# Performance work log

Hardware: AMD Instinct MI355X
Metric: run time of the kernel (lower is better)

The kernel has to match this reference:

```python
import jax, jax.numpy as jnp
import numpy as np

N_NODES = 20000
N_EDGES = 320000
IN_DIM = 256
OUT_DIM = 256
NUM_RELS = 8
NUM_BASES = 4


def setup_inputs() -> dict:
    key = jax.random.key(0)
    k = jax.random.split(key, 7)
    return {
        "h": jax.random.normal(k[0], (N_NODES, IN_DIM), dtype=jnp.float32),
        "basis": jax.random.normal(k[1], (NUM_BASES, IN_DIM, OUT_DIM), dtype=jnp.float32)
        * (6.0 / (IN_DIM + OUT_DIM)) ** 0.5,
        "w_comp": jax.random.normal(k[2], (NUM_RELS, NUM_BASES), dtype=jnp.float32),
        "bias": jax.random.normal(k[3], (OUT_DIM,), dtype=jnp.float32) * 0.01,
        "src": jax.random.randint(k[4], (N_EDGES,), 0, N_NODES, dtype=jnp.int32),
        "dst": jax.random.randint(k[5], (N_EDGES,), 0, N_NODES, dtype=jnp.int32),
        "etype": jax.random.randint(k[6], (N_EDGES,), 0, NUM_RELS, dtype=jnp.int32),
    }


def reference(h, basis, w_comp, bias, src, dst, etype):
    # Faithful to the torch basis-decomposition quirk:
    #   weight.view(in, B, out); matmul(w_comp, .) -> [in, R, out]; view -> [R, in, out]
    in_dim, out_dim = h.shape[1], basis.shape[2]
    num_rels = w_comp.shape[0]
    wr = basis.reshape(in_dim, NUM_BASES, out_dim)          # raw-buffer reinterpret (torch .view)
    weight = jnp.einsum("rb,ibo->iro", w_comp, wr)          # [in, R, out]
    weight = weight.reshape(num_rels, in_dim, out_dim)      # raw-buffer reinterpret (torch .view)

    # msg_e = h[src_e] @ weight[etype_e]. Group by relation: transform all nodes
    # under every relation weight (dense GEMMs), then gather per edge.
    t = jnp.einsum("nd,rdo->rno", h, weight)                # [R, N, out]
    msg = t[etype, src]                                     # [E, out]

    # scatter-sum aggregation to destination nodes (dgl fn.sum)
    agg = jax.ops.segment_sum(msg, dst, num_segments=h.shape[0])  # [N, out]
    return jax.nn.relu(agg + bias)
```

## Files before the change

kernel.cpp:

```cpp
#include <hip/hip_runtime.h>


#define N_NODES  20000
#define N_EDGES  320000
#define IN_DIM   256
#define OUT_DIM  256
#define NUM_RELS 8
#define KDIM     128
#define M_PAD    20032
#define CAP      96

#define FOLD_BLOCKS 2500
#define FILL_BLOCKS 1250
#define BP_BLOCKS   128

typedef __attribute__((ext_vector_type(8)))  short short8;
typedef __attribute__((ext_vector_type(16))) float float16v;

static __device__ __forceinline__ unsigned f2bf_rne(float x) {
    unsigned u = __float_as_uint(x);
    return (u + 0x7fffu + ((u >> 16) & 1u)) >> 16;
}
static __device__ __forceinline__ float bf2f(unsigned b) {
    return __uint_as_float(b << 16);
}

__global__ __launch_bounds__(256)
void prep_kernel(const float* __restrict__ h, const float* __restrict__ w_comp,
                 unsigned short* __restrict__ U,
                 const int* __restrict__ src, const int* __restrict__ dst,
                 const int* __restrict__ et,
                 int* __restrict__ cnt, int* __restrict__ bucket,
                 const float* __restrict__ basis, unsigned short* __restrict__ Bp) {
    int b = blockIdx.x;
    int t = threadIdx.x;
    if (b < FOLD_BLOCKS) {
        int gid = b * 256 + t;
        int n = gid >> 5, k = gid & 31;
        const float* hp = h + (size_t)n * IN_DIM + k * 8;
        float4 h0 = *(const float4*)hp;
        float4 h1 = *(const float4*)(hp + 4);
        float hv[8] = {h0.x, h0.y, h0.z, h0.w, h1.x, h1.y, h1.z, h1.w};
        float a0 = 0.f, a1 = 0.f, a2 = 0.f, a3 = 0.f;
#pragma unroll
        for (int j = 0; j < 8; ++j) {
            float hj = hv[j];
            a0 += hj * w_comp[j * 4 + 0];
            a1 += hj * w_comp[j * 4 + 1];
            a2 += hj * w_comp[j * 4 + 2];
            a3 += hj * w_comp[j * 4 + 3];
        }
        uint2 p;
        p.x = f2bf_rne(a0) | (f2bf_rne(a1) << 16);
        p.y = f2bf_rne(a2) | (f2bf_rne(a3) << 16);
        *(uint2*)(U + ((size_t)n << 7) + k * 4) = p;
    } else if (b < FOLD_BLOCKS + FILL_BLOCKS) {
        int e = (b - FOLD_BLOCKS) * 256 + t;
        int d = dst[e];
        int p = atomicAdd(&cnt[d], 1);
        if (p < CAP) bucket[(size_t)d * CAP + p] = src[e] | (et[e] << 16);
    } else {
        int frag = (b - FOLD_BLOCKS - FILL_BLOCKS) * 256 + t;
        int lane = frag & 63;
        int ks   = (frag >> 6) & 7;
        int r    = (frag >> 9) & 7;
        int ct   = frag >> 12;
        int o  = ct * 32 + (lane & 31);
        int kb = r * 128 + ks * 16 + (lane >> 5) * 8;
        const float* bsp = basis + (size_t)kb * 256 + o;
        unsigned v[8];
#pragma unroll
        for (int j = 0; j < 8; ++j) v[j] = f2bf_rne(bsp[(size_t)j * 256]);
        uint4 p;
        p.x = v[0] | (v[1] << 16);
        p.y = v[2] | (v[3] << 16);
        p.z = v[4] | (v[5] << 16);
        p.w = v[6] | (v[7] << 16);
        *(uint4*)(Bp + (size_t)frag * 8) = p;
    }
}

__global__ __launch_bounds__(256)
void aggregate_kernel(const unsigned short* __restrict__ U,
                      const int* __restrict__ cnt,
                      const int* __restrict__ bucket,
                      unsigned int* __restrict__ S) {
    int wid  = threadIdx.x >> 6;
    int lane = threadIdx.x & 63;
    int d = blockIdx.x * 4 + wid;
    float2 acc[NUM_RELS];
#pragma unroll
    for (int r = 0; r < NUM_RELS; ++r) { acc[r].x = 0.f; acc[r].y = 0.f; }

    if (d < N_NODES) {
        int n = cnt[d];
        if (n > CAP) n = CAP;
        const int4* bp4 = (const int4*)(bucket + (size_t)d * CAP);
        int4 e4 = bp4[0];
        for (int i = 0; i < n; i += 4) {
            int4 cur = e4;
            e4 = bp4[(i >> 2) + 1];
            int m = n - i;
            int es[4] = {cur.x, cur.y, cur.z, cur.w};
#pragma unroll
            for (int j = 0; j < 4; ++j) {
                if (j < m) {
                    int e = es[j];
                    int s = e & 0xffff;
                    int r = __builtin_amdgcn_readfirstlane(e >> 16);
                    unsigned u = *(const unsigned*)(U + ((size_t)s << 7) + lane * 2);
                    float fx = bf2f(u & 0xffffu), fy = bf2f(u >> 16);
                    switch (r) {
                        case 0: acc[0].x += fx; acc[0].y += fy; break;
                        case 1: acc[1].x += fx; acc[1].y += fy; break;
                        case 2: acc[2].x += fx; acc[2].y += fy; break;
                        case 3: acc[3].x += fx; acc[3].y += fy; break;
                        case 4: acc[4].x += fx; acc[4].y += fy; break;
                        case 5: acc[5].x += fx; acc[5].y += fy; break;
                        case 6: acc[6].x += fx; acc[6].y += fy; break;
                        default: acc[7].x += fx; acc[7].y += fy; break;
                    }
                }
            }
        }
    }
#pragma unroll
    for (int r = 0; r < NUM_RELS; ++r) {
        unsigned p = f2bf_rne(acc[r].x) | (f2bf_rne(acc[r].y) << 16);
        S[(((size_t)r * M_PAD + d) << 6) + lane] = p;
    }
}

__global__ __launch_bounds__(512)
void gemm_kernel(const unsigned short* __restrict__ S,
                 const unsigned short* __restrict__ Bp,
                 const float* __restrict__ bias,
                 float* __restrict__ out) {
    __shared__ unsigned short At[32][136];
    int t = threadIdx.x;
    int w = t >> 6, lane = t & 63;
    int ln = lane & 31, hi = lane >> 5;
    int n0 = blockIdx.x * 32;
    int c0 = w * 32;

    int srow = t >> 4, sq = t & 15;
    const unsigned short* sbase = S + (((size_t)n0 + srow) << 7) + sq * 8;
    uint4 pre = *(const uint4*)sbase;

    float16v acc = {};

    for (int r = 0; r < NUM_RELS; ++r) {
        if (r > 0) __syncthreads();
        *(uint4*)&At[srow][sq * 8] = pre;
        __syncthreads();
        if (r + 1 < NUM_RELS)
            pre = *(const uint4*)(sbase + (((size_t)(r + 1) * M_PAD) << 7));
        const unsigned short* bpr = Bp + (((size_t)(w * 8 + r) * 8) << 9) + lane * 8;
#pragma unroll
        for (int ks = 0; ks < 8; ++ks) {
            short8 a  = *(const short8*)&At[ln][ks * 16 + hi * 8];
            short8 bo = *(const short8*)(bpr + (ks << 9));
            acc = __builtin_amdgcn_mfma_f32_32x32x16_bf16(a, bo, acc, 0, 0, 0);
        }
    }

    float bs = bias[c0 + ln];
#pragma unroll
    for (int reg = 0; reg < 16; ++reg) {
        int row = (reg & 3) + 8 * (reg >> 2) + 4 * hi;
        int n = n0 + row;
        if (n < N_NODES)
            out[(size_t)n * OUT_DIM + c0 + ln] = fmaxf(acc[reg] + bs, 0.f);
    }
}

extern "C" void kernel_launch(void* const* d_in, const int* in_sizes, int n_in,
                              void* d_out, int out_size, void* d_ws, size_t ws_size,
                              hipStream_t stream) {
    const float* h      = (const float*)d_in[0];
    const float* basis  = (const float*)d_in[1];
    const float* w_comp = (const float*)d_in[2];
    const float* bias   = (const float*)d_in[3];
    const int*   src    = (const int*)d_in[4];
    const int*   dst    = (const int*)d_in[5];
    const int*   etype  = (const int*)d_in[6];
    float*       out    = (float*)d_out;

    char* ws = (char*)d_ws;
    size_t off = 0;
    unsigned short* U   = (unsigned short*)(ws + off); off += (size_t)N_NODES * KDIM * 2;
    unsigned int*   S   = (unsigned int*)(ws + off);   off += (size_t)NUM_RELS * M_PAD * KDIM * 2;
    unsigned short* Bp  = (unsigned short*)(ws + off); off += (size_t)8 * 8 * 8 * 64 * 8 * 2;
    int* cnt    = (int*)(ws + off); off += (size_t)M_PAD * 4;
    int* bucket = (int*)(ws + off); off += ((size_t)M_PAD * CAP + 16) * 4;

    hipMemsetAsync(cnt, 0, (size_t)N_NODES * 4, stream);

    prep_kernel<<<FOLD_BLOCKS + FILL_BLOCKS + BP_BLOCKS, 256, 0, stream>>>(
        h, w_comp, U, src, dst, etype, cnt, bucket, basis, Bp);

    aggregate_kernel<<<M_PAD / 4, 256, 0, stream>>>(U, cnt, bucket, S);

    gemm_kernel<<<M_PAD / 32, 512, 0, stream>>>((const unsigned short*)S, Bp, bias, out);
}
```

Measured before the change: 152.4 us.

## Fuse edge aggregation into relation GEMM via shared-memory accumulation tile

Merges the aggregation and GEMM kernels so each 512-thread block gathers edge features for its 32 destination nodes into a per-relation bf16 tile in shared memory, then runs the MFMA GEMM directly from it. This removes the large global intermediate S (write and re-read) and one kernel launch. In exchange, each wave processes four nodes serially, uses many more accumulator registers, and the large shared-memory tile limits blocks per CU, which can reduce latency hiding for the irregular gathers.

```diff
diff --git a/kernel.cpp b/kernel.cpp
--- a/kernel.cpp
+++ b/kernel.cpp
@@ -13,6 +13,8 @@
 #define FOLD_BLOCKS 2500
 #define FILL_BLOCKS 1250
 #define BP_BLOCKS   128
+
+#define SROW 1096
 
 typedef __attribute__((ext_vector_type(8)))  short short8;
 typedef __attribute__((ext_vector_type(16))) float float16v;
@@ -80,87 +82,83 @@
     }
 }
 
-__global__ __launch_bounds__(256)
-void aggregate_kernel(const unsigned short* __restrict__ U,
-                      const int* __restrict__ cnt,
-                      const int* __restrict__ bucket,
-                      unsigned int* __restrict__ S) {
-    int wid  = threadIdx.x >> 6;
-    int lane = threadIdx.x & 63;
-    int d = blockIdx.x * 4 + wid;
-    float2 acc[NUM_RELS];
-#pragma unroll
-    for (int r = 0; r < NUM_RELS; ++r) { acc[r].x = 0.f; acc[r].y = 0.f; }
-
-    if (d < N_NODES) {
-        int n = cnt[d];
-        if (n > CAP) n = CAP;
-        const int4* bp4 = (const int4*)(bucket + (size_t)d * CAP);
-        int4 e4 = bp4[0];
-        for (int i = 0; i < n; i += 4) {
-            int4 cur = e4;
-            e4 = bp4[(i >> 2) + 1];
-            int m = n - i;
-            int es[4] = {cur.x, cur.y, cur.z, cur.w};
-#pragma unroll
-            for (int j = 0; j < 4; ++j) {
-                if (j < m) {
-                    int e = es[j];
-                    int s = e & 0xffff;
-                    int r = __builtin_amdgcn_readfirstlane(e >> 16);
-                    unsigned u = *(const unsigned*)(U + ((size_t)s << 7) + lane * 2);
-                    float fx = bf2f(u & 0xffffu), fy = bf2f(u >> 16);
-                    switch (r) {
-                        case 0: acc[0].x += fx; acc[0].y += fy; break;
-                        case 1: acc[1].x += fx; acc[1].y += fy; break;
-                        case 2: acc[2].x += fx; acc[2].y += fy; break;
-                        case 3: acc[3].x += fx; acc[3].y += fy; break;
-                        case 4: acc[4].x += fx; acc[4].y += fy; break;
-                        case 5: acc[5].x += fx; acc[5].y += fy; break;
-                        case 6: acc[6].x += fx; acc[6].y += fy; break;
-                        default: acc[7].x += fx; acc[7].y += fy; break;
-                    }
-                }
-            }
-        }
-    }
-#pragma unroll
-    for (int r = 0; r < NUM_RELS; ++r) {
-        unsigned p = f2bf_rne(acc[r].x) | (f2bf_rne(acc[r].y) << 16);
-        S[(((size_t)r * M_PAD + d) << 6) + lane] = p;
-    }
-}
-
 __global__ __launch_bounds__(512)
-void gemm_kernel(const unsigned short* __restrict__ S,
-                 const unsigned short* __restrict__ Bp,
-                 const float* __restrict__ bias,
-                 float* __restrict__ out) {
-    __shared__ unsigned short At[32][136];
+void agemm_kernel(const unsigned short* __restrict__ U,
+                  const int* __restrict__ cnt,
+                  const int* __restrict__ bucket,
+                  const unsigned short* __restrict__ Bp,
+                  const float* __restrict__ bias,
+                  float* __restrict__ out) {
+    __shared__ unsigned short Sacc[32][SROW];
     int t = threadIdx.x;
     int w = t >> 6, lane = t & 63;
     int ln = lane & 31, hi = lane >> 5;
     int n0 = blockIdx.x * 32;
+
+    float2 acc[4][NUM_RELS];
+#pragma unroll
+    for (int i = 0; i < 4; ++i)
+#pragma unroll
+        for (int r = 0; r < NUM_RELS; ++r) { acc[i][r].x = 0.f; acc[i][r].y = 0.f; }
+
+#pragma unroll
+    for (int i = 0; i < 4; ++i) {
+        int d = n0 + w * 4 + i;
+        if (d < N_NODES) {
+            int n = cnt[d];
+            if (n > CAP) n = CAP;
+            const int4* bp4 = (const int4*)(bucket + (size_t)d * CAP);
+            int4 e4 = bp4[0];
+            for (int ii = 0; ii < n; ii += 4) {
+                int4 cur = e4;
+                e4 = bp4[(ii >> 2) + 1];
+                int m = n - ii;
+                int es[4] = {cur.x, cur.y, cur.z, cur.w};
+#pragma unroll
+                for (int j = 0; j < 4; ++j) {
+                    if (j < m) {
+                        int e = es[j];
+                        int s = e & 0xffff;
+                        int r = __builtin_amdgcn_readfirstlane(e >> 16);
+                        unsigned u = *(const unsigned*)(U + ((size_t)s << 7) + lane * 2);
+                        float fx = bf2f(u & 0xffffu), fy = bf2f(u >> 16);
+                        switch (r) {
+                            case 0: acc[i][0].x += fx; acc[i][0].y += fy; break;
+                            case 1: acc[i][1].x += fx; acc[i][1].y += fy; break;
+                            case 2: acc[i][2].x += fx; acc[i][2].y += fy; break;
+                            case 3: acc[i][3].x += fx; acc[i][3].y += fy; break;
+                            case 4: acc[i][4].x += fx; acc[i][4].y += fy; break;
+                            case 5: acc[i][5].x += fx; acc[i][5].y += fy; break;
+                            case 6: acc[i][6].x += fx; acc[i][6].y += fy; break;
+                            default: acc[i][7].x += fx; acc[i][7].y += fy; break;
+                        }
+                    }
+                }
+            }
+        }
+    }
+
+#pragma unroll
+    for (int i = 0; i < 4; ++i) {
+        int dl = w * 4 + i;
+#pragma unroll
+        for (int r = 0; r < NUM_RELS; ++r) {
+            unsigned p = f2bf_rne(acc[i][r].x) | (f2bf_rne(acc[i][r].y) << 16);
+            *(unsigned*)&Sacc[dl][r * 136 + lane * 2] = p;
+        }
+    }
+    __syncthreads();
+
     int c0 = w * 32;
-
-    int srow = t >> 4, sq = t & 15;
-    const unsigned short* sbase = S + (((size_t)n0 + srow) << 7) + sq * 8;
-    uint4 pre = *(const uint4*)sbase;
-
-    float16v acc = {};
-
+    float16v facc = {};
+#pragma unroll
     for (int r = 0; r < NUM_RELS; ++r) {
-        if (r > 0) __syncthreads();
-        *(uint4*)&At[srow][sq * 8] = pre;
-        __syncthreads();
-        if (r + 1 < NUM_RELS)
-            pre = *(const uint4*)(sbase + (((size_t)(r + 1) * M_PAD) << 7));
         const unsigned short* bpr = Bp + (((size_t)(w * 8 + r) * 8) << 9) + lane * 8;
 #pragma unroll
         for (int ks = 0; ks < 8; ++ks) {
-            short8 a  = *(const short8*)&At[ln][ks * 16 + hi * 8];
+            short8 a  = *(const short8*)&Sacc[ln][r * 136 + ks * 16 + hi * 8];
             short8 bo = *(const short8*)(bpr + (ks << 9));
-            acc = __builtin_amdgcn_mfma_f32_32x32x16_bf16(a, bo, acc, 0, 0, 0);
+            facc = __builtin_amdgcn_mfma_f32_32x32x16_bf16(a, bo, facc, 0, 0, 0);
         }
     }
 
@@ -170,7 +168,7 @@
         int row = (reg & 3) + 8 * (reg >> 2) + 4 * hi;
         int n = n0 + row;
         if (n < N_NODES)
-            out[(size_t)n * OUT_DIM + c0 + ln] = fmaxf(acc[reg] + bs, 0.f);
+            out[(size_t)n * OUT_DIM + c0 + ln] = fmaxf(facc[reg] + bs, 0.f);
     }
 }
 
@@ -189,7 +187,6 @@
     char* ws = (char*)d_ws;
     size_t off = 0;
     unsigned short* U   = (unsigned short*)(ws + off); off += (size_t)N_NODES * KDIM * 2;
-    unsigned int*   S   = (unsigned int*)(ws + off);   off += (size_t)NUM_RELS * M_PAD * KDIM * 2;
     unsigned short* Bp  = (unsigned short*)(ws + off); off += (size_t)8 * 8 * 8 * 64 * 8 * 2;
     int* cnt    = (int*)(ws + off); off += (size_t)M_PAD * 4;
     int* bucket = (int*)(ws + off); off += ((size_t)M_PAD * CAP + 16) * 4;
@@ -199,7 +196,5 @@
     prep_kernel<<<FOLD_BLOCKS + FILL_BLOCKS + BP_BLOCKS, 256, 0, stream>>>(
         h, w_comp, U, src, dst, etype, cnt, bucket, basis, Bp);
 
-    aggregate_kernel<<<M_PAD / 4, 256, 0, stream>>>(U, cnt, bucket, S);
-
-    gemm_kernel<<<M_PAD / 32, 512, 0, stream>>>((const unsigned short*)S, Bp, bias, out);
-}
+    agemm_kernel<<<M_PAD / 32, 512, 0, stream>>>(U, cnt, bucket, Bp, bias, out);
+}
```

Measured after the change: 183.2 us. 1.2x slower.
